# Optimization experiments

Measured on AMD Instinct MI355X. Metric: run time of the kernel, lower is better.

The kernel has to match this reference:

```python
import jax, jax.numpy as jnp
import numpy as np

NX, NY, NZ = 64, 48, 32          # grid_resolution
N = NX * NY * NZ                 # 98304 grid cells
P = 10                           # neighbors_in_radius
D = 3                            # spatial dims
M = 5                            # num_modes (fourier)
BN = 64                          # base_neurons
BN_IN = 8                        # base_neurons_in (output channels)
IN_FEAT = D * (1 + 2 * M)        # 33


def _linear_init(k, fan_in, fan_out):
    s = 1.0 / np.sqrt(fan_in)
    kw, kb = jax.random.split(k)
    W = jax.random.uniform(kw, (fan_in, fan_out), jnp.float32, -s, s)
    b = jax.random.uniform(kb, (fan_out,), jnp.float32, -s, s)
    return W, b


def setup_inputs() -> dict:
    key = jax.random.key(0)
    ks = jax.random.split(key, 6)
    # neighbor point coordinates gathered by ball query: (b, N, P, 3)
    x = jax.random.normal(ks[0], (1, N, P, D), jnp.float32)
    # regular grid coordinates: (b, nx, ny, nz, 3)
    grid = jax.random.normal(ks[1], (1, NX, NY, NZ, D), jnp.float32)
    # fourier frequency buffer: exp(linspace(0, pi, num_modes))
    freqs = jnp.exp(jnp.linspace(0.0, float(np.pi), M)).astype(jnp.float32)
    W1, b1 = _linear_init(ks[2], IN_FEAT, BN)
    W2, b2 = _linear_init(ks[3], BN, BN // 2)
    W3, b3 = _linear_init(ks[4], BN // 2, BN_IN)
    return dict(x=x, grid=grid, freqs=freqs,
                W1=W1, b1=b1, W2=W2, b2=b2, W3=W3, b3=b3)


def _fourier_encode(coords, freqs):
    # coords: (b, N, P, D), freqs: (F,)
    scaled = coords[..., None, :] * freqs[:, None]          # (b, N, P, F, D)
    b, n, p = coords.shape[:3]
    scaled = scaled.reshape(b, n, p, -1)                    # (b, N, P, F*D)
    return jnp.concatenate([jnp.sin(scaled), jnp.cos(scaled)], axis=-1)


def reference(x, grid, freqs, W1, b1, W2, b2, W3, b3):
    gelu = lambda t: jax.nn.gelu(t, approximate=False)  # torch F.gelu default = exact erf
    # Fourier feature encode neighbor coords: (b, N, P, 33)
    facets = jnp.concatenate([x, _fourier_encode(x, freqs)], axis=-1)
    h = gelu(facets @ W1 + b1)                              # (b, N, P, 64)
    h = gelu(h @ W2 + b2)                                   # (b, N, P, 32)
    h = jnp.tanh(h @ W3 + b3)                               # (b, N, P, 8)
    # mask out padded neighbors (zero coords); original uses x-coordinate channel
    mask = (jnp.abs(x[..., 0:1]) > 1e-6).astype(h.dtype)    # (b, N, P, 1)
    out = jnp.sum(h * mask, axis=2)                         # scatter/aggregate -> (b, N, 8)
    out = out.reshape(out.shape[0], NX, NY, NZ, BN_IN)
    return jnp.transpose(out, (0, 4, 1, 2, 3))              # (b, 8, nx, ny, nz)
```

## Files before the change

kernel.cpp:

```cpp
#include <hip/hip_runtime.h>
#include <math.h>

#define NXD 64
#define NYD 48
#define NZD 32
#define NPT (NXD*NYD*NZD)
#define PN  10
#define MF  5
#define H1  64
#define H2  32
#define H3  8

#define PTS_PER_BLOCK 32
#define ROWS_PER_BLOCK (PTS_PER_BLOCK*PN)
#define TILES_PER_WAVE 5

#define A2S 72
#define A3S 40

#define INV2PI 0.15915494309189535f

typedef __attribute__((ext_vector_type(8))) _Float16 half8;
typedef __attribute__((ext_vector_type(2))) _Float16 half2v;
typedef __attribute__((ext_vector_type(2))) __fp16   fp16x2;
typedef __attribute__((ext_vector_type(2))) short    shortv2;
typedef __attribute__((ext_vector_type(4))) float    f32x4;

__device__ __forceinline__ half2v cvt_pk_h2(float lo, float hi) {
    fp16x2 p = __builtin_amdgcn_cvt_pkrtz(lo, hi);
    return __builtin_bit_cast(half2v, p);
}

static __device__ const unsigned short kSlotTab[32] = {
  2048,    3,   70,  137,  204,  271, 1042, 1109,
  2561, 1176, 1243, 1310,  516,  583,  650,  717,
  2562,  272, 1043, 1110, 1177, 1244, 1311,  517,
    72,  139,  206,  273, 1044, 1111, 1178, 1245 };

__device__ __forceinline__ _Float16 exp2h(_Float16 v) {
    _Float16 r;
    asm("v_exp_f16 %0, %1" : "=v"(r) : "v"(v));
    return r;
}

__device__ __forceinline__ half2v gelu_pk(float lo, float hi) {
    const _Float16 C1 = (_Float16)2.3022082f, C2 = (_Float16)0.10294324f;
    const half2v x  = cvt_pk_h2(lo, hi);
    const half2v x2 = x * x;
    half2v t = x * __builtin_elementwise_fma(x2, (half2v){C2, C2}, (half2v){C1, C1});
    t = __builtin_elementwise_min(t, (half2v){(_Float16)14.0f, (_Float16)14.0f});
    const _Float16 e0 = exp2h(t[0]);
    const _Float16 e1 = exp2h(t[1]);
    const half2v one = {(_Float16)1.0f, (_Float16)1.0f};
    const half2v two = {(_Float16)2.0f, (_Float16)2.0f};
    const half2v y = (half2v){e0, e1} + one;
    const shortv2 rb = (shortv2){(short)0x7800, (short)0x7800} - __builtin_bit_cast(shortv2, y);
    half2v r = __builtin_bit_cast(half2v, rb);
    r = r * __builtin_elementwise_fma(-y, r, two);
    r = r * __builtin_elementwise_fma(-y, r, two);
    return x - x * r;
}

__device__ __forceinline__ float tanh_fast(float v) {
    float E = __builtin_amdgcn_exp2f(2.8853901f * v);
    return 1.0f - 2.0f * __builtin_amdgcn_rcpf(E + 1.0f);
}

__global__ __launch_bounds__(256) void domino_mfma_kernel(
    const float* __restrict__ x,
    const float* __restrict__ freqs,
    const float* __restrict__ W1,
    const float* __restrict__ b1,
    const float* __restrict__ W2,
    const float* __restrict__ b2,
    const float* __restrict__ W3,
    const float* __restrict__ b3,
    float* __restrict__ out)
{
    __shared__ __align__(16) _Float16 a2buf[4][16 * A2S];
    __shared__ __align__(16) float cbuf[976];
    __shared__ __align__(16) _Float16 obuf[ROWS_PER_BLOCK * 9];
    __shared__ __align__(16) float mcx[4][16];
    __shared__ __align__(16) float mv32[4][16];
    __shared__ __align__(16) float coefA[2][32];
    __shared__ __align__(16) float coefB[2][32];
    __shared__ __align__(16) float coefO[2][32];

    const int tid  = threadIdx.x;
    const int w    = tid >> 6;
    const int lane = tid & 63;
    const int lr   = lane & 15;
    const int lg   = lane >> 4;

    const int wrow0 = blockIdx.x * ROWS_PER_BLOCK + w * (TILES_PER_WAVE*16);

    if (tid < 32) {
        const unsigned e = kSlotTab[tid];
        const int m = (e >> 6) & 7, path = (e >> 9) & 1, ty = (e >> 10) & 3;
        const float fm = freqs[m] * INV2PI;
        const float fa = (ty != 2 && path == 0) ? fm : 0.0f;
        const float fb = (ty != 2 && path == 1) ? fm : 0.0f;
        const float fo = (ty == 1) ? 0.25f : 0.0f;
        coefA[0][tid] = fa; coefA[1][tid] = fa;
        coefB[0][tid] = fb; coefB[1][tid] = fb;
        coefO[0][tid] = fo; coefO[1][tid] = fo;
    }

    {
        const int sl = (w == 3 && lane >= 60) ? 59 : lane;
        const float* gsrc = x + (size_t)wrow0 * 3 + (size_t)sl * 4;
        __builtin_amdgcn_global_load_lds(
            (const __attribute__((address_space(1))) void*)gsrc,
            (__attribute__((address_space(3))) void*)&cbuf[w * 240], 16, 0, 0);
    }

    const float f4rev = freqs[4] * INV2PI;
    const float rawf  = (lg < 3) ? 1.0f : 0.0f;

    half8 B1f[4];
    float  w32[4], bv1[4];
    #pragma unroll
    for (int t1 = 0; t1 < 4; ++t1) {
        #pragma unroll
        for (int j = 0; j < 8; ++j) {
            const int row = kSlotTab[lg*8 + j] & 63;
            B1f[t1][j] = (_Float16)W1[row*H1 + t1*16 + lr];
        }
        w32[t1] = W1[32*H1 + t1*16 + lr];
        bv1[t1] = b1[t1*16 + lr];
    }
    half8 B2f[2][2];
    float  bv2[2];
    #pragma unroll
    for (int s = 0; s < 2; ++s)
        #pragma unroll
        for (int t2 = 0; t2 < 2; ++t2)
            #pragma unroll
            for (int j = 0; j < 8; ++j)
                B2f[s][t2][j] = (_Float16)W2[(s*32 + lg*8 + j)*H2 + t2*16 + lr];
    #pragma unroll
    for (int t2 = 0; t2 < 2; ++t2) bv2[t2] = b2[t2*16 + lr];

    half8 B3f;
    float  bv3 = (lr < H3) ? b3[lr] : 0.0f;
    #pragma unroll
    for (int j = 0; j < 8; ++j)
        B3f[j] = (lr < H3) ? (_Float16)W3[(lg*8 + j)*H3 + lr] : (_Float16)0.0f;

    __syncthreads();

    #pragma unroll 1
    for (int t = 0; t < TILES_PER_WAVE; ++t) {
        const int cfx = w*240 + (t*16 + lr)*3;
        const float cx = cbuf[cfx + 0];
        const float cy = cbuf[cfx + 1];
        const float cz = cbuf[cfx + 2];

        const float cA = (lg <= 1) ? cx : ((lg == 2) ? cy : cz);
        const float cB = (lg == 0) ? cx : ((lg == 1) ? cy : cz);

        const int tc = t & 1;
        float fv[8];
        {
            const f32x4 fa0 = *(const f32x4*)&coefA[tc][lg*8];
            const f32x4 fb0 = *(const f32x4*)&coefB[tc][lg*8];
            const f32x4 fo0 = *(const f32x4*)&coefO[tc][lg*8];
            #pragma unroll
            for (int j = 0; j < 4; ++j) {
                float rev = cA*fa0[j] + (cB*fb0[j] + fo0[j]);
                fv[j] = __builtin_amdgcn_sinf(__builtin_amdgcn_fractf(rev));
            }
        }
        __builtin_amdgcn_sched_barrier(0);
        {
            const f32x4 fa1 = *(const f32x4*)&coefA[tc][lg*8 + 4];
            const f32x4 fb1 = *(const f32x4*)&coefB[tc][lg*8 + 4];
            const f32x4 fo1 = *(const f32x4*)&coefO[tc][lg*8 + 4];
            #pragma unroll
            for (int j = 0; j < 4; ++j) {
                float rev = cA*fa1[j] + (cB*fb1[j] + fo1[j]);
                fv[4+j] = __builtin_amdgcn_sinf(__builtin_amdgcn_fractf(rev));
            }
        }
        fv[0] += rawf * (cB - fv[0]);

        if (lg == 0) {
            mcx[w][lr]  = cx;
            mv32[w][lr] = __builtin_amdgcn_sinf(__builtin_amdgcn_fractf(cz * f4rev + 0.25f));
        }

        union { half2v h2[4]; half8 h8; } a1u;
        #pragma unroll
        for (int j = 0; j < 4; ++j)
            a1u.h2[j] = cvt_pk_h2(fv[2*j], fv[2*j+1]);
        const half8 a1 = a1u.h8;

        f32x4 c1[4];
        #pragma unroll
        for (int t1 = 0; t1 < 4; ++t1) {
            f32x4 ci = {bv1[t1], bv1[t1], bv1[t1], bv1[t1]};
            c1[t1] = __builtin_amdgcn_mfma_f32_16x16x32_f16(a1, B1f[t1], ci, 0, 0, 0);
        }
        const f32x4 v32r = *(const f32x4*)&mv32[w][lg*4];
        const f32x4 mxr  = *(const f32x4*)&mcx[w][lg*4];
        #pragma unroll
        for (int t1 = 0; t1 < 4; ++t1)
            #pragma unroll
            for (int r = 0; r < 4; ++r)
                c1[t1][r] += v32r[r] * w32[t1];

        #pragma unroll
        for (int t1 = 0; t1 < 4; ++t1) {
            const half2v g01 = gelu_pk(c1[t1][0], c1[t1][1]);
            const half2v g23 = gelu_pk(c1[t1][2], c1[t1][3]);
            const int col = t1*16 + lr;
            a2buf[w][(lg*4 + 0)*A2S + col] = g01[0];
            a2buf[w][(lg*4 + 1)*A2S + col] = g01[1];
            a2buf[w][(lg*4 + 2)*A2S + col] = g23[0];
            a2buf[w][(lg*4 + 3)*A2S + col] = g23[1];
        }
        half8 a2f[2];
        #pragma unroll
        for (int s = 0; s < 2; ++s)
            a2f[s] = *(const half8*)&a2buf[w][lr*A2S + s*32 + lg*8];

        f32x4 c2[2];
        #pragma unroll
        for (int t2 = 0; t2 < 2; ++t2) {
            f32x4 ci = {bv2[t2], bv2[t2], bv2[t2], bv2[t2]};
            ci = __builtin_amdgcn_mfma_f32_16x16x32_f16(a2f[0], B2f[0][t2], ci, 0, 0, 0);
            c2[t2] = __builtin_amdgcn_mfma_f32_16x16x32_f16(a2f[1], B2f[1][t2], ci, 0, 0, 0);
        }

        _Float16* const a3p = &a2buf[w][0];
        #pragma unroll
        for (int t2 = 0; t2 < 2; ++t2) {
            const half2v g01 = gelu_pk(c2[t2][0], c2[t2][1]);
            const half2v g23 = gelu_pk(c2[t2][2], c2[t2][3]);
            const int col = t2*16 + lr;
            a3p[(lg*4 + 0)*A3S + col] = g01[0];
            a3p[(lg*4 + 1)*A3S + col] = g01[1];
            a3p[(lg*4 + 2)*A3S + col] = g23[0];
            a3p[(lg*4 + 3)*A3S + col] = g23[1];
        }
        half8 a3f = *(const half8*)&a3p[lr*A3S + lg*8];

        f32x4 c3 = {bv3, bv3, bv3, bv3};
        c3 = __builtin_amdgcn_mfma_f32_16x16x32_f16(a3f, B3f, c3, 0, 0, 0);

        #pragma unroll
        for (int r = 0; r < 4; ++r) {
            const int brow = w*(TILES_PER_WAVE*16) + t*16 + lg*4 + r;
            const float mk = (fabsf(mxr[r]) > 1e-6f) ? 1.0f : 0.0f;
            if (lr < H3) obuf[brow*9 + lr] = (_Float16)(mk * tanh_fast(c3[r]));
        }
    }

    __syncthreads();

    {
        const int p  = tid >> 3;
        const int ch = tid & 7;
        float sum = 0.0f;
        #pragma unroll
        for (int i = 0; i < PN; ++i) sum += (float)obuf[(p*PN + i)*9 + ch];
        const int gp = blockIdx.x * PTS_PER_BLOCK + p;
        out[(size_t)ch * NPT + gp] = sum;
    }
}

extern "C" void kernel_launch(void* const* d_in, const int* in_sizes, int n_in,
                              void* d_out, int out_size, void* d_ws, size_t ws_size,
                              hipStream_t stream) {
    const float* x     = (const float*)d_in[0];
    const float* freqs = (const float*)d_in[2];
    const float* W1    = (const float*)d_in[3];
    const float* b1    = (const float*)d_in[4];
    const float* W2    = (const float*)d_in[5];
    const float* b2    = (const float*)d_in[6];
    const float* W3    = (const float*)d_in[7];
    const float* b3    = (const float*)d_in[8];
    float* out = (float*)d_out;

    const int grid = NPT / PTS_PER_BLOCK;
    domino_mfma_kernel<<<grid, 256, 0, stream>>>(x, freqs, W1, b1, W2, b2, W3, b3, out);
}
```

Measured before the change: 120.9 us.

## Chain MLP layers in registers via transposed MFMA and process multiple chunks per block

Swaps the MFMA operand order so each layer's output fragment already sits in the layout the next layer needs as its B operand. The LDS round trips through a2buf, mcx and mv32 go away, and the weight and bias loads are reordered to match. Each block now handles three chunks, double-buffering coordinate staging with global_load_lds so weight loading and setup are amortised and the next chunk's load overlaps compute. The cost is fewer blocks (1024), more barriers per block, and a repeated v32 sine in every lane.

```diff
diff --git a/kernel.cpp b/kernel.cpp
--- a/kernel.cpp
+++ b/kernel.cpp
@@ -12,11 +12,9 @@
 #define H3  8
 
 #define PTS_PER_BLOCK 32
+#define CHUNKS 3
 #define ROWS_PER_BLOCK (PTS_PER_BLOCK*PN)
 #define TILES_PER_WAVE 5
-
-#define A2S 72
-#define A3S 40
 
 #define INV2PI 0.15915494309189535f
 
@@ -77,11 +75,8 @@
     const float* __restrict__ b3,
     float* __restrict__ out)
 {
-    __shared__ __align__(16) _Float16 a2buf[4][16 * A2S];
-    __shared__ __align__(16) float cbuf[976];
+    __shared__ __align__(16) float cbuf[2][976];
     __shared__ __align__(16) _Float16 obuf[ROWS_PER_BLOCK * 9];
-    __shared__ __align__(16) float mcx[4][16];
-    __shared__ __align__(16) float mv32[4][16];
     __shared__ __align__(16) float coefA[2][32];
     __shared__ __align__(16) float coefB[2][32];
     __shared__ __align__(16) float coefO[2][32];
@@ -92,7 +87,14 @@
     const int lr   = lane & 15;
     const int lg   = lane >> 4;
 
-    const int wrow0 = blockIdx.x * ROWS_PER_BLOCK + w * (TILES_PER_WAVE*16);
+    auto stage_coords = [&](int c, int buf) {
+        const int row0 = (blockIdx.x*CHUNKS + c) * ROWS_PER_BLOCK + w*(TILES_PER_WAVE*16);
+        const int sl = (w == 3 && lane >= 60) ? 59 : lane;
+        const float* gsrc = x + (size_t)row0 * 3 + (size_t)sl * 4;
+        __builtin_amdgcn_global_load_lds(
+            (const __attribute__((address_space(1))) void*)gsrc,
+            (__attribute__((address_space(3))) void*)&cbuf[buf][w * 240], 16, 0, 0);
+    };
 
     if (tid < 32) {
         const unsigned e = kSlotTab[tid];
@@ -106,19 +108,13 @@
         coefO[0][tid] = fo; coefO[1][tid] = fo;
     }
 
-    {
-        const int sl = (w == 3 && lane >= 60) ? 59 : lane;
-        const float* gsrc = x + (size_t)wrow0 * 3 + (size_t)sl * 4;
-        __builtin_amdgcn_global_load_lds(
-            (const __attribute__((address_space(1))) void*)gsrc,
-            (__attribute__((address_space(3))) void*)&cbuf[w * 240], 16, 0, 0);
-    }
+    stage_coords(0, 0);
 
     const float f4rev = freqs[4] * INV2PI;
     const float rawf  = (lg < 3) ? 1.0f : 0.0f;
 
     half8 B1f[4];
-    float  w32[4], bv1[4];
+    f32x4 w32s[4], bv1s[4];
     #pragma unroll
     for (int t1 = 0; t1 < 4; ++t1) {
         #pragma unroll
@@ -126,146 +122,139 @@
             const int row = kSlotTab[lg*8 + j] & 63;
             B1f[t1][j] = (_Float16)W1[row*H1 + t1*16 + lr];
         }
-        w32[t1] = W1[32*H1 + t1*16 + lr];
-        bv1[t1] = b1[t1*16 + lr];
+        #pragma unroll
+        for (int r = 0; r < 4; ++r) {
+            w32s[t1][r] = W1[32*H1 + t1*16 + lg*4 + r];
+            bv1s[t1][r] = b1[t1*16 + lg*4 + r];
+        }
     }
     half8 B2f[2][2];
-    float  bv2[2];
-    #pragma unroll
-    for (int s = 0; s < 2; ++s)
+    f32x4 bv2s[2];
+    #pragma unroll
+    for (int q = 0; q < 2; ++q)
         #pragma unroll
         for (int t2 = 0; t2 < 2; ++t2)
             #pragma unroll
             for (int j = 0; j < 8; ++j)
-                B2f[s][t2][j] = (_Float16)W2[(s*32 + lg*8 + j)*H2 + t2*16 + lr];
-    #pragma unroll
-    for (int t2 = 0; t2 < 2; ++t2) bv2[t2] = b2[t2*16 + lr];
+                B2f[q][t2][j] = (_Float16)W2[((2*q + (j>>2))*16 + lg*4 + (j&3))*H2 + t2*16 + lr];
+    #pragma unroll
+    for (int t2 = 0; t2 < 2; ++t2)
+        #pragma unroll
+        for (int r = 0; r < 4; ++r)
+            bv2s[t2][r] = b2[t2*16 + lg*4 + r];
 
     half8 B3f;
-    float  bv3 = (lr < H3) ? b3[lr] : 0.0f;
     #pragma unroll
     for (int j = 0; j < 8; ++j)
-        B3f[j] = (lr < H3) ? (_Float16)W3[(lg*8 + j)*H3 + lr] : (_Float16)0.0f;
+        B3f[j] = (lr < H3) ? (_Float16)W3[((j>>2)*16 + lg*4 + (j&3))*H3 + lr] : (_Float16)0.0f;
+    f32x4 bv3s;
+    #pragma unroll
+    for (int r = 0; r < 4; ++r)
+        bv3s[r] = (lg < 2) ? b3[lg*4 + r] : 0.0f;
 
     __syncthreads();
 
     #pragma unroll 1
-    for (int t = 0; t < TILES_PER_WAVE; ++t) {
-        const int cfx = w*240 + (t*16 + lr)*3;
-        const float cx = cbuf[cfx + 0];
-        const float cy = cbuf[cfx + 1];
-        const float cz = cbuf[cfx + 2];
-
-        const float cA = (lg <= 1) ? cx : ((lg == 2) ? cy : cz);
-        const float cB = (lg == 0) ? cx : ((lg == 1) ? cy : cz);
-
-        const int tc = t & 1;
-        float fv[8];
+    for (int c = 0; c < CHUNKS; ++c) {
+        if (c + 1 < CHUNKS) stage_coords(c + 1, (c + 1) & 1);
+        const float* cbp = &cbuf[c & 1][0];
+
+        #pragma unroll 1
+        for (int t = 0; t < TILES_PER_WAVE; ++t) {
+            const int tc = t & 1;
+            const int cfx = w*240 + (t*16 + lr)*3;
+            const float cx = cbp[cfx + 0];
+            const float cy = cbp[cfx + 1];
+            const float cz = cbp[cfx + 2];
+            const float cA = (lg <= 1) ? cx : ((lg == 2) ? cy : cz);
+            const float cB = (lg == 0) ? cx : ((lg == 1) ? cy : cz);
+
+            float fv[8];
+            {
+                const f32x4 fa0 = *(const f32x4*)&coefA[tc][lg*8];
+                const f32x4 fb0 = *(const f32x4*)&coefB[tc][lg*8];
+                const f32x4 fo0 = *(const f32x4*)&coefO[tc][lg*8];
+                #pragma unroll
+                for (int j = 0; j < 4; ++j) {
+                    float rev = cA*fa0[j] + (cB*fb0[j] + fo0[j]);
+                    fv[j] = __builtin_amdgcn_sinf(__builtin_amdgcn_fractf(rev));
+                }
+                const f32x4 fa1 = *(const f32x4*)&coefA[tc][lg*8 + 4];
+                const f32x4 fb1 = *(const f32x4*)&coefB[tc][lg*8 + 4];
+                const f32x4 fo1 = *(const f32x4*)&coefO[tc][lg*8 + 4];
+                #pragma unroll
+                for (int j = 0; j < 4; ++j) {
+                    float rev = cA*fa1[j] + (cB*fb1[j] + fo1[j]);
+                    fv[4+j] = __builtin_amdgcn_sinf(__builtin_amdgcn_fractf(rev));
+                }
+            }
+            fv[0] += rawf * (cB - fv[0]);
+
+            const float v32 = __builtin_amdgcn_sinf(__builtin_amdgcn_fractf(cz * f4rev + 0.25f));
+
+            union { half2v h2[4]; half8 h8; } a1u;
+            #pragma unroll
+            for (int j = 0; j < 4; ++j)
+                a1u.h2[j] = cvt_pk_h2(fv[2*j], fv[2*j+1]);
+            const half8 a1 = a1u.h8;
+
+            f32x4 c1[4];
+            #pragma unroll
+            for (int t1 = 0; t1 < 4; ++t1)
+                c1[t1] = __builtin_amdgcn_mfma_f32_16x16x32_f16(B1f[t1], a1, bv1s[t1], 0, 0, 0);
+            #pragma unroll
+            for (int t1 = 0; t1 < 4; ++t1)
+                #pragma unroll
+                for (int r = 0; r < 4; ++r)
+                    c1[t1][r] += v32 * w32s[t1][r];
+
+            union { half2v h2[4]; half8 h8; } a2u0, a2u1;
+            a2u0.h2[0] = gelu_pk(c1[0][0], c1[0][1]);
+            a2u0.h2[1] = gelu_pk(c1[0][2], c1[0][3]);
+            a2u0.h2[2] = gelu_pk(c1[1][0], c1[1][1]);
+            a2u0.h2[3] = gelu_pk(c1[1][2], c1[1][3]);
+            a2u1.h2[0] = gelu_pk(c1[2][0], c1[2][1]);
+            a2u1.h2[1] = gelu_pk(c1[2][2], c1[2][3]);
+            a2u1.h2[2] = gelu_pk(c1[3][0], c1[3][1]);
+            a2u1.h2[3] = gelu_pk(c1[3][2], c1[3][3]);
+
+            f32x4 c2[2];
+            #pragma unroll
+            for (int t2 = 0; t2 < 2; ++t2) {
+                f32x4 ci = __builtin_amdgcn_mfma_f32_16x16x32_f16(B2f[0][t2], a2u0.h8, bv2s[t2], 0, 0, 0);
+                c2[t2]   = __builtin_amdgcn_mfma_f32_16x16x32_f16(B2f[1][t2], a2u1.h8, ci, 0, 0, 0);
+            }
+
+            union { half2v h2[4]; half8 h8; } a3u;
+            a3u.h2[0] = gelu_pk(c2[0][0], c2[0][1]);
+            a3u.h2[1] = gelu_pk(c2[0][2], c2[0][3]);
+            a3u.h2[2] = gelu_pk(c2[1][0], c2[1][1]);
+            a3u.h2[3] = gelu_pk(c2[1][2], c2[1][3]);
+
+            f32x4 c3 = __builtin_amdgcn_mfma_f32_16x16x32_f16(B3f, a3u.h8, bv3s, 0, 0, 0);
+
+            const float mk = (fabsf(cx) > 1e-6f) ? 1.0f : 0.0f;
+            if (lg < 2) {
+                const int base = (w*(TILES_PER_WAVE*16) + t*16 + lr)*9 + lg*4;
+                #pragma unroll
+                for (int r = 0; r < 4; ++r)
+                    obuf[base + r] = (_Float16)(mk * tanh_fast(c3[r]));
+            }
+        }
+
+        __syncthreads();
+
         {
-            const f32x4 fa0 = *(const f32x4*)&coefA[tc][lg*8];
-            const f32x4 fb0 = *(const f32x4*)&coefB[tc][lg*8];
-            const f32x4 fo0 = *(const f32x4*)&coefO[tc][lg*8];
-            #pragma unroll
-            for (int j = 0; j < 4; ++j) {
-                float rev = cA*fa0[j] + (cB*fb0[j] + fo0[j]);
-                fv[j] = __builtin_amdgcn_sinf(__builtin_amdgcn_fractf(rev));
-            }
-        }
-        __builtin_amdgcn_sched_barrier(0);
-        {
-            const f32x4 fa1 = *(const f32x4*)&coefA[tc][lg*8 + 4];
-            const f32x4 fb1 = *(const f32x4*)&coefB[tc][lg*8 + 4];
-            const f32x4 fo1 = *(const f32x4*)&coefO[tc][lg*8 + 4];
-            #pragma unroll
-            for (int j = 0; j < 4; ++j) {
-                float rev = cA*fa1[j] + (cB*fb1[j] + fo1[j]);
-                fv[4+j] = __builtin_amdgcn_sinf(__builtin_amdgcn_fractf(rev));
-            }
-        }
-        fv[0] += rawf * (cB - fv[0]);
-
-        if (lg == 0) {
-            mcx[w][lr]  = cx;
-            mv32[w][lr] = __builtin_amdgcn_sinf(__builtin_amdgcn_fractf(cz * f4rev + 0.25f));
-        }
-
-        union { half2v h2[4]; half8 h8; } a1u;
-        #pragma unroll
-        for (int j = 0; j < 4; ++j)
-            a1u.h2[j] = cvt_pk_h2(fv[2*j], fv[2*j+1]);
-        const half8 a1 = a1u.h8;
-
-        f32x4 c1[4];
-        #pragma unroll
-        for (int t1 = 0; t1 < 4; ++t1) {
-            f32x4 ci = {bv1[t1], bv1[t1], bv1[t1], bv1[t1]};
-            c1[t1] = __builtin_amdgcn_mfma_f32_16x16x32_f16(a1, B1f[t1], ci, 0, 0, 0);
-        }
-        const f32x4 v32r = *(const f32x4*)&mv32[w][lg*4];
-        const f32x4 mxr  = *(const f32x4*)&mcx[w][lg*4];
-        #pragma unroll
-        for (int t1 = 0; t1 < 4; ++t1)
-            #pragma unroll
-            for (int r = 0; r < 4; ++r)
-                c1[t1][r] += v32r[r] * w32[t1];
-
-        #pragma unroll
-        for (int t1 = 0; t1 < 4; ++t1) {
-            const half2v g01 = gelu_pk(c1[t1][0], c1[t1][1]);
-            const half2v g23 = gelu_pk(c1[t1][2], c1[t1][3]);
-            const int col = t1*16 + lr;
-            a2buf[w][(lg*4 + 0)*A2S + col] = g01[0];
-            a2buf[w][(lg*4 + 1)*A2S + col] = g01[1];
-            a2buf[w][(lg*4 + 2)*A2S + col] = g23[0];
-            a2buf[w][(lg*4 + 3)*A2S + col] = g23[1];
-        }
-        half8 a2f[2];
-        #pragma unroll
-        for (int s = 0; s < 2; ++s)
-            a2f[s] = *(const half8*)&a2buf[w][lr*A2S + s*32 + lg*8];
-
-        f32x4 c2[2];
-        #pragma unroll
-        for (int t2 = 0; t2 < 2; ++t2) {
-            f32x4 ci = {bv2[t2], bv2[t2], bv2[t2], bv2[t2]};
-            ci = __builtin_amdgcn_mfma_f32_16x16x32_f16(a2f[0], B2f[0][t2], ci, 0, 0, 0);
-            c2[t2] = __builtin_amdgcn_mfma_f32_16x16x32_f16(a2f[1], B2f[1][t2], ci, 0, 0, 0);
-        }
-
-        _Float16* const a3p = &a2buf[w][0];
-        #pragma unroll
-        for (int t2 = 0; t2 < 2; ++t2) {
-            const half2v g01 = gelu_pk(c2[t2][0], c2[t2][1]);
-            const half2v g23 = gelu_pk(c2[t2][2], c2[t2][3]);
-            const int col = t2*16 + lr;
-            a3p[(lg*4 + 0)*A3S + col] = g01[0];
-            a3p[(lg*4 + 1)*A3S + col] = g01[1];
-            a3p[(lg*4 + 2)*A3S + col] = g23[0];
-            a3p[(lg*4 + 3)*A3S + col] = g23[1];
-        }
-        half8 a3f = *(const half8*)&a3p[lr*A3S + lg*8];
-
-        f32x4 c3 = {bv3, bv3, bv3, bv3};
-        c3 = __builtin_amdgcn_mfma_f32_16x16x32_f16(a3f, B3f, c3, 0, 0, 0);
-
-        #pragma unroll
-        for (int r = 0; r < 4; ++r) {
-            const int brow = w*(TILES_PER_WAVE*16) + t*16 + lg*4 + r;
-            const float mk = (fabsf(mxr[r]) > 1e-6f) ? 1.0f : 0.0f;
-            if (lr < H3) obuf[brow*9 + lr] = (_Float16)(mk * tanh_fast(c3[r]));
-        }
-    }
-
-    __syncthreads();
-
-    {
-        const int p  = tid >> 3;
-        const int ch = tid & 7;
-        float sum = 0.0f;
-        #pragma unroll
-        for (int i = 0; i < PN; ++i) sum += (float)obuf[(p*PN + i)*9 + ch];
-        const int gp = blockIdx.x * PTS_PER_BLOCK + p;
-        out[(size_t)ch * NPT + gp] = sum;
+            const int p  = tid >> 3;
+            const int ch = tid & 7;
+            float sum = 0.0f;
+            #pragma unroll
+            for (int i = 0; i < PN; ++i) sum += (float)obuf[(p*PN + i)*9 + ch];
+            const int gp = blockIdx.x * (PTS_PER_BLOCK*CHUNKS) + c*PTS_PER_BLOCK + p;
+            out[(size_t)ch * NPT + gp] = sum;
+        }
+
+        if (c + 1 < CHUNKS) __syncthreads();
     }
 }
 
@@ -282,6 +271,6 @@
     const float* b3    = (const float*)d_in[8];
     float* out = (float*)d_out;
 
-    const int grid = NPT / PTS_PER_BLOCK;
+    const int grid = NPT / (PTS_PER_BLOCK * CHUNKS);
     domino_mfma_kernel<<<grid, 256, 0, stream>>>(x, freqs, W1, b1, W2, b2, W3, b3, out);
 }
```

After: 121.2 us. About the same (+0.3%).
